# Performance work log

Hardware: AMD Instinct MI355X
Metric: run time of the kernel (lower is better)

The kernel has to match this reference:

```python
import jax, jax.numpy as jnp
from jax import lax
import numpy as np

K_SIZE = 3  # SteerableKernelBase.create_radial(3)


def _radial_basis_3x3():
    """Orthonormal radial steerable basis on a 3x3 grid.
    Returns 6 unit-norm kernels: [k0_center, k0_ring, k1_cos, k1_sin, k2_cos, k2_sin]."""
    ys, xs = np.mgrid[-1:2, -1:2].astype(np.float32)
    ang = np.arctan2(ys, xs)
    ring = (np.hypot(xs, ys) > 0).astype(np.float32)

    def unit(k):
        return (k / np.linalg.norm(k)).astype(np.float32)

    b0c = np.zeros((3, 3), np.float32); b0c[1, 1] = 1.0
    basis = np.stack([
        b0c,                       # k=0, r=0
        unit(ring),                # k=0, r=1
        unit(np.cos(ang) * ring),  # k=1 real
        unit(np.sin(ang) * ring),  # k=1 imag
        unit(np.cos(2 * ang) * ring),  # k=2 real
        unit(np.sin(2 * ang) * ring),  # k=2 imag
    ])
    return jnp.asarray(basis)  # (6, 3, 3)


def setup_inputs() -> dict:
    key = jax.random.key(0)
    k1, k2, k3 = jax.random.split(key, 3)
    N, C_in, C_out, H, W = 16, 64, 64, 128, 128
    x = jax.random.normal(k1, (N, C_in, H, W), dtype=jnp.float32)
    # steering angle field in [0,1); alpha = (cos 2*pi*theta, sin 2*pi*theta) is unitary
    theta = jax.random.uniform(k2, (N, 1, H, W), dtype=jnp.float32)
    # steerable weights: (n_out, n_in, 4) -> [k0 center, k0 ring, k1, k2]
    fan_in = C_in * K_SIZE * K_SIZE
    std = jnp.sqrt(2.0 / fan_in)  # relu gain init as in steerable_base.init_weights
    weights = jax.random.normal(k3, (C_out, C_in, 4), dtype=jnp.float32) * std
    bias = jnp.zeros((C_out,), dtype=jnp.float32)
    return {"x": x, "theta": theta, "weights": weights, "bias": bias}


def reference(x, theta, weights, bias):
    basis = _radial_basis_3x3()  # (6,3,3)
    O = weights.shape[0]
    w = weights[..., None, None]  # (O,I,4,1,1)
    # Synthesize per-harmonic kernels (O,I,3,3) from the steerable basis
    k0 = w[:, :, 0] * basis[0] + w[:, :, 1] * basis[1]
    k1r = w[:, :, 2] * basis[2]
    k1i = w[:, :, 2] * basis[3]
    k2r = w[:, :, 3] * basis[4]
    k2i = w[:, :, 3] * basis[5]
    ker = jnp.concatenate([k0, k1r, k1i, k2r, k2i], axis=0)  # (5O, I, 3, 3)

    z = lax.conv_general_dilated(
        x, ker, window_strides=(1, 1), padding="SAME",
        dimension_numbers=("NCHW", "OIHW", "NCHW"))  # (N, 5O, H, W)
    N, _, H, W = z.shape
    z = z.reshape(N, 5, O, H, W)

    # angle harmonics cos(k*alpha), sin(k*alpha); alpha unitary so rho=1 path
    a = 2.0 * jnp.pi * theta  # (N,1,H,W)
    c1, s1 = jnp.cos(a), jnp.sin(a)
    c2 = 2.0 * c1 * c1 - 1.0
    s2 = 2.0 * s1 * c1

    out = (z[:, 0] + c1 * z[:, 1] + s1 * z[:, 2]
           + c2 * z[:, 3] + s2 * z[:, 4])
    return out + bias[None, :, None, None]
```

## Files before the change

### kernel.cpp

```cpp
#include <hip/hip_runtime.h>


typedef __bf16 bf16x8 __attribute__((ext_vector_type(8)));
typedef float  f32x16 __attribute__((ext_vector_type(16)));
typedef float  f32x4  __attribute__((ext_vector_type(4)));
typedef unsigned int u32;
typedef const __attribute__((address_space(1))) u32* gp_t;
typedef __attribute__((address_space(3))) u32* lp_t;

#define HH 128
#define WW 128
#define CHCH 8
#define NCHUNK 8
#define NBUF 3
#define RROWS 10
#define RCOLS 40
#define CHF 400
#define CHIMG 65536

__global__ void wt_repack(const float* __restrict__ wt,
                          unsigned short* __restrict__ wb) {
    int i = blockIdx.x * 256 + threadIdx.x;
    int o = i >> 8, k = i & 255;
    union { float f; u32 u; } v; v.f = wt[i];
    unsigned short b = (unsigned short)((v.u + 0x7FFF + ((v.u >> 16) & 1)) >> 16);
    int kcg = k >> 4, hxx = (k >> 3) & 1, r = k & 7;
    wb[((kcg * 2 + hxx) * 64 + o) * 8 + r] = b;
}

__global__ __launch_bounds__(256, 3) void steered_conv_mfma(
    const float* __restrict__ x, const float* __restrict__ theta,
    const unsigned short* __restrict__ wb, const float* __restrict__ bias,
    float* __restrict__ out)
{
    __shared__ __attribute__((aligned(16))) float lds[NBUF][CHCH][CHF];

    const int tid = threadIdx.x;
    const int wid = tid >> 6, lane = tid & 63;
    const int pc = lane & 31, hx = lane >> 5;

    const int bb = blockIdx.x;
    const int swz = (bb & 7) * 128 + (bb >> 3);
    const int n = swz >> 6;
    const int ty = (swz >> 2) & 15, tx = swz & 3;
    const int h0 = ty * 8, w0 = tx * 32;
    const int p0 = wid * 2;

    const int oA = lane * 16;
    const int rA = oA / 160;
    const int cA = oA - rA * 160;
    int ghA = h0 - 1 + rA; ghA = ghA < 0 ? 0 : (ghA > 127 ? 127 : ghA);
    int srcA = ghA * 512 + w0 * 4 - 16 + cA;
    srcA = srcA < 0 ? 0 : srcA;
    const bool skA = (w0 == 0 && cA < 16) || (w0 == 96 && cA >= 144)
                   || (h0 == 0 && rA == 0);

    const int oB = 1024 + lane * 16;
    const int rB = oB / 160;
    const int cB = oB - rB * 160;
    int ghB = h0 - 1 + rB; ghB = ghB < 0 ? 0 : (ghB > 127 ? 127 : ghB);
    int srcB = ghB * 512 + w0 * 4 - 16 + cB;
    srcB = srcB < 0 ? 0 : (srcB > CHIMG - 16 ? CHIMG - 16 : srcB);
    const bool skB = (lane >= 36) || (w0 == 0 && cB < 16) || (w0 == 96 && cB >= 144)
                   || (h0 == 120 && rB == 9);

    const char* xn = (const char*)x + (size_t)n * 64 * CHIMG;

    float s1a, c1a, s1b, c1b;
    __sincosf(6.2831853071795864769f * theta[(n*HH + h0+p0)*WW + w0+pc], &s1a, &c1a);
    __sincosf(6.2831853071795864769f * theta[(n*HH + h0+p0+1)*WW + w0+pc], &s1b, &c1b);
    const float c2a = 2.f*c1a*c1a - 1.f, s2a = 2.f*s1a*c1a;
    const float c2b = 2.f*c1b*c1b - 1.f, s2b = 2.f*s1b*c1b;

    if ((h0 == 0) | (h0 == 120) | (w0 == 0) | (w0 == 96)) {
        f32x4* z = (f32x4*)&lds[0][0][0];
        for (int i = tid; i < NBUF * CHCH * CHF / 4; i += 256)
            z[i] = f32x4{0.f, 0.f, 0.f, 0.f};
    }
    __syncthreads();

    auto stage = [&](int t) {
        const char* xc = xn + (size_t)(t * CHCH) * CHIMG;
        #pragma unroll
        for (int j = 0; j < 2; ++j) {
            const int ch = wid * 2 + j;
            const char* s = xc + ch * CHIMG;
            char* d = (char*)&lds[t % NBUF][ch][0];
            if (!skA) __builtin_amdgcn_global_load_lds((gp_t)(s + srcA), (lp_t)d, 16, 0, 0);
            if (!skB) __builtin_amdgcn_global_load_lds((gp_t)(s + srcB), (lp_t)(d + 1024), 16, 0, 0);
        }
    };

    const unsigned short* wbl = wb + (hx * 64 + pc) * 8;
    bf16x8 wE0, wE1, wE2, wE3, wO0, wO1, wO2, wO3;

    stage(0);
    {
        const unsigned short* wr = wbl;
        wE0 = *(const bf16x8*)(wr);
        wE1 = *(const bf16x8*)(wr + 256);
        wE2 = *(const bf16x8*)(wr + 1024);
        wE3 = *(const bf16x8*)(wr + 1280);
    }
    stage(1);

    f32x16 acc00, acc01, acc10, acc11;
    #pragma unroll
    for (int r = 0; r < 16; ++r) { acc00[r]=0.f; acc01[r]=0.f; acc10[r]=0.f; acc11[r]=0.f; }

    const float RS  = 0.35355339059327373f;
    const float HMR = 0.14644660940672627f;

    #pragma unroll
    for (int c = 0; c < NCHUNK; ++c) {
        if (c == NCHUNK - 1) asm volatile("s_waitcnt vmcnt(0)" ::: "memory");
        else                 asm volatile("s_waitcnt vmcnt(4)" ::: "memory");
        __builtin_amdgcn_sched_barrier(0);
        __builtin_amdgcn_s_barrier();
        if (c + 1 < NCHUNK) {
            const unsigned short* wr = wbl + (c + 1) * 2048;
            if ((c + 1) & 1) {
                wO0 = *(const bf16x8*)(wr);
                wO1 = *(const bf16x8*)(wr + 256);
                wO2 = *(const bf16x8*)(wr + 1024);
                wO3 = *(const bf16x8*)(wr + 1280);
            } else {
                wE0 = *(const bf16x8*)(wr);
                wE1 = *(const bf16x8*)(wr + 256);
                wE2 = *(const bf16x8*)(wr + 1024);
                wE3 = *(const bf16x8*)(wr + 1280);
            }
        }
        if (c + 2 < NCHUNK) stage(c + 2);
        __builtin_amdgcn_sched_barrier(0);

        const bf16x8 A00 = (c & 1) ? wO0 : wE0;
        const bf16x8 A01 = (c & 1) ? wO1 : wE1;
        const bf16x8 A10 = (c & 1) ? wO2 : wE2;
        const bf16x8 A11 = (c & 1) ? wO3 : wE3;

        const float* tb = &lds[c % NBUF][0][p0 * RCOLS + pc + 3];
        #pragma unroll
        for (int kc = 0; kc < 2; ++kc) {
            bf16x8 b0, b1;
            #pragma unroll
            for (int cs = 0; cs < 2; ++cs) {
                const float* t = tb + (kc * 4 + hx * 2 + cs) * CHF;
                const float t00=t[0],   t01=t[1],   t02=t[2];
                const float t10=t[40],  t11=t[41],  t12=t[42];
                const float t20=t[80],  t21=t[81],  t22=t[82];
                const float t30=t[120], t31=t[121], t32=t[122];
                const float S0=t00+t01+t02, S1=t10+t11+t12;
                const float S2=t20+t21+t22, S3=t30+t31+t32;
                const float D0=t02-t00, D1=t12-t10, D2=t22-t20, D3=t32-t30;
                {
                    const float F1 = RS * (S0 + S2 + S1 - t11);
                    const float B2 = RS * (D0 + D2) + 0.5f * D1;
                    const float B3 = RS * (S2 - S0) + HMR * (t21 - t01);
                    const float B4 = 0.5f * (S1 - t11 - t01 - t21);
                    const float B5 = 0.5f * (D2 - D0);
                    b0[cs*4+0] = (__bf16)t11;
                    b0[cs*4+1] = (__bf16)F1;
                    b0[cs*4+2] = (__bf16)(c1a * B2 + s1a * B3);
                    b0[cs*4+3] = (__bf16)(c2a * B4 + s2a * B5);
                }
                {
                    const float F1 = RS * (S1 + S3 + S2 - t21);
                    const float B2 = RS * (D1 + D3) + 0.5f * D2;
                    const float B3 = RS * (S3 - S1) + HMR * (t31 - t11);
                    const float B4 = 0.5f * (S2 - t21 - t11 - t31);
                    const float B5 = 0.5f * (D3 - D1);
                    b1[cs*4+0] = (__bf16)t21;
                    b1[cs*4+1] = (__bf16)F1;
                    b1[cs*4+2] = (__bf16)(c1b * B2 + s1b * B3);
                    b1[cs*4+3] = (__bf16)(c2b * B4 + s2b * B5);
                }
            }
            const bf16x8 A0 = kc ? A10 : A00;
            const bf16x8 A1 = kc ? A11 : A01;
            __builtin_amdgcn_s_setprio(1);
            acc00 = __builtin_amdgcn_mfma_f32_32x32x16_bf16(A0, b0, acc00, 0, 0, 0);
            acc01 = __builtin_amdgcn_mfma_f32_32x32x16_bf16(A1, b0, acc01, 0, 0, 0);
            acc10 = __builtin_amdgcn_mfma_f32_32x32x16_bf16(A0, b1, acc10, 0, 0, 0);
            acc11 = __builtin_amdgcn_mfma_f32_32x32x16_bf16(A1, b1, acc11, 0, 0, 0);
            __builtin_amdgcn_s_setprio(0);
        }
    }

    const size_t hw = (size_t)HH * WW;
    float* op = out + (size_t)n * 64 * hw + (size_t)(h0 + p0) * WW + w0 + pc;
    #pragma unroll
    for (int r = 0; r < 16; ++r) {
        const int o = (r & 3) + 8 * (r >> 2) + 4 * hx;
        const float bo = bias[o], bo2 = bias[o + 32];
        op[(size_t)o * hw]             = acc00[r] + bo;
        op[(size_t)(o + 32) * hw]      = acc01[r] + bo2;
        op[(size_t)o * hw + WW]        = acc10[r] + bo;
        op[(size_t)(o + 32) * hw + WW] = acc11[r] + bo2;
    }
}

extern "C" void kernel_launch(void* const* d_in, const int* in_sizes, int n_in,
                              void* d_out, int out_size, void* d_ws, size_t ws_size,
                              hipStream_t stream) {
    const float* x     = (const float*)d_in[0];
    const float* theta = (const float*)d_in[1];
    const float* wt    = (const float*)d_in[2];
    const float* bias  = (const float*)d_in[3];
    float* out = (float*)d_out;
    unsigned short* wb = (unsigned short*)d_ws;

    wt_repack<<<64, 256, 0, stream>>>(wt, wb);

    steered_conv_mfma<<<1024, 256, 0, stream>>>(x, theta, wb, bias, out);
}
```

Baseline: 41.84 us.

## Use single-wave blocks with private double-buffered LDS, removing block barriers

Measured after the change: 41.03 us. Within noise of the previous version (-1.9%).

```diff
diff --git a/kernel.cpp b/kernel.cpp
--- a/kernel.cpp
+++ b/kernel.cpp
@@ -10,12 +10,7 @@
 
 #define HH 128
 #define WW 128
-#define CHCH 8
-#define NCHUNK 8
-#define NBUF 3
-#define RROWS 10
-#define RCOLS 40
-#define CHF 400
+#define HW 16384
 #define CHIMG 65536
 
 __global__ void wt_repack(const float* __restrict__ wt,
@@ -28,73 +23,72 @@
     wb[((kcg * 2 + hxx) * 64 + o) * 8 + r] = b;
 }
 
-__global__ __launch_bounds__(256, 3) void steered_conv_mfma(
+__global__ __launch_bounds__(64, 3) void steered_conv_mfma(
     const float* __restrict__ x, const float* __restrict__ theta,
     const unsigned short* __restrict__ wb, const float* __restrict__ bias,
     float* __restrict__ out)
 {
-    __shared__ __attribute__((aligned(16))) float lds[NBUF][CHCH][CHF];
-
-    const int tid = threadIdx.x;
-    const int wid = tid >> 6, lane = tid & 63;
+    __shared__ __attribute__((aligned(16))) float xs[2][8][4][40];
+
+    const int lane = threadIdx.x & 63;
     const int pc = lane & 31, hx = lane >> 5;
 
-    const int bb = blockIdx.x;
-    const int swz = (bb & 7) * 128 + (bb >> 3);
-    const int n = swz >> 6;
-    const int ty = (swz >> 2) & 15, tx = swz & 3;
-    const int h0 = ty * 8, w0 = tx * 32;
-    const int p0 = wid * 2;
-
-    const int oA = lane * 16;
-    const int rA = oA / 160;
-    const int cA = oA - rA * 160;
-    int ghA = h0 - 1 + rA; ghA = ghA < 0 ? 0 : (ghA > 127 ? 127 : ghA);
-    int srcA = ghA * 512 + w0 * 4 - 16 + cA;
-    srcA = srcA < 0 ? 0 : srcA;
-    const bool skA = (w0 == 0 && cA < 16) || (w0 == 96 && cA >= 144)
-                   || (h0 == 0 && rA == 0);
-
-    const int oB = 1024 + lane * 16;
-    const int rB = oB / 160;
-    const int cB = oB - rB * 160;
-    int ghB = h0 - 1 + rB; ghB = ghB < 0 ? 0 : (ghB > 127 ? 127 : ghB);
-    int srcB = ghB * 512 + w0 * 4 - 16 + cB;
-    srcB = srcB < 0 ? 0 : (srcB > CHIMG - 16 ? CHIMG - 16 : srcB);
-    const bool skB = (lane >= 36) || (w0 == 0 && cB < 16) || (w0 == 96 && cB >= 144)
-                   || (h0 == 120 && rB == 9);
+    const int bb  = blockIdx.x;
+    const int swz = (bb & 7) * 512 + (bb >> 3);
+    const int n   = swz >> 8;
+    const int rem = swz & 255;
+    const int hA  = (rem >> 2) * 2;
+    const int w0  = (rem & 3) * 32;
+    const int w   = w0 + pc;
+
+    int soff[5];
+    int skip[5];
+    #pragma unroll
+    for (int d = 0; d < 5; ++d) {
+        const int i   = d * 1024 + lane * 16;
+        const int ch  = i / 640;
+        const int rm  = i - ch * 640;
+        const int row = rm / 160;
+        const int c16 = rm - row * 160;
+        const int gh  = hA - 1 + row;
+        const int ghc = gh < 0 ? 0 : (gh > 127 ? 127 : gh);
+        int so = ch * CHIMG + ghc * 512 + w0 * 4 - 16 + c16;
+        soff[d] = so < 0 ? 0 : so;
+        skip[d] = (gh < 0) | (gh > 127) |
+                  ((w0 == 0) & (c16 < 16)) | ((w0 == 96) & (c16 >= 144));
+    }
 
     const char* xn = (const char*)x + (size_t)n * 64 * CHIMG;
 
     float s1a, c1a, s1b, c1b;
-    __sincosf(6.2831853071795864769f * theta[(n*HH + h0+p0)*WW + w0+pc], &s1a, &c1a);
-    __sincosf(6.2831853071795864769f * theta[(n*HH + h0+p0+1)*WW + w0+pc], &s1b, &c1b);
+    __sincosf(6.2831853071795864769f * theta[(n*HH + hA)*WW + w], &s1a, &c1a);
+    __sincosf(6.2831853071795864769f * theta[(n*HH + hA+1)*WW + w], &s1b, &c1b);
     const float c2a = 2.f*c1a*c1a - 1.f, s2a = 2.f*s1a*c1a;
     const float c2b = 2.f*c1b*c1b - 1.f, s2b = 2.f*s1b*c1b;
 
-    if ((h0 == 0) | (h0 == 120) | (w0 == 0) | (w0 == 96)) {
-        f32x4* z = (f32x4*)&lds[0][0][0];
-        for (int i = tid; i < NBUF * CHCH * CHF / 4; i += 256)
-            z[i] = f32x4{0.f, 0.f, 0.f, 0.f};
-    }
-    __syncthreads();
+    if (hA == 0 || hA == 126 || w0 == 0 || w0 == 96) {
+        f32x4* z = (f32x4*)&xs[0][0][0][0];
+        #pragma unroll
+        for (int i = 0; i < 10; ++i)
+            z[lane + i * 64] = f32x4{0.f, 0.f, 0.f, 0.f};
+        asm volatile("s_waitcnt lgkmcnt(0)" ::: "memory");
+    }
 
     auto stage = [&](int t) {
-        const char* xc = xn + (size_t)(t * CHCH) * CHIMG;
+        const char* sb = xn + (size_t)(t * 8) * CHIMG;
+        char* db = (char*)&xs[t & 1][0][0][0];
         #pragma unroll
-        for (int j = 0; j < 2; ++j) {
-            const int ch = wid * 2 + j;
-            const char* s = xc + ch * CHIMG;
-            char* d = (char*)&lds[t % NBUF][ch][0];
-            if (!skA) __builtin_amdgcn_global_load_lds((gp_t)(s + srcA), (lp_t)d, 16, 0, 0);
-            if (!skB) __builtin_amdgcn_global_load_lds((gp_t)(s + srcB), (lp_t)(d + 1024), 16, 0, 0);
-        }
+        for (int d = 0; d < 5; ++d)
+            if (!skip[d])
+                __builtin_amdgcn_global_load_lds((gp_t)(sb + soff[d]),
+                                                 (lp_t)(db + d * 1024), 16, 0, 0);
     };
 
     const unsigned short* wbl = wb + (hx * 64 + pc) * 8;
     bf16x8 wE0, wE1, wE2, wE3, wO0, wO1, wO2, wO3;
 
     stage(0);
+    __builtin_amdgcn_sched_barrier(0);
     {
         const unsigned short* wr = wbl;
         wE0 = *(const bf16x8*)(wr);
@@ -102,7 +96,9 @@
         wE2 = *(const bf16x8*)(wr + 1024);
         wE3 = *(const bf16x8*)(wr + 1280);
     }
+    __builtin_amdgcn_sched_barrier(0);
     stage(1);
+    __builtin_amdgcn_sched_barrier(0);
 
     f32x16 acc00, acc01, acc10, acc11;
     #pragma unroll
@@ -112,12 +108,11 @@
     const float HMR = 0.14644660940672627f;
 
     #pragma unroll
-    for (int c = 0; c < NCHUNK; ++c) {
-        if (c == NCHUNK - 1) asm volatile("s_waitcnt vmcnt(0)" ::: "memory");
-        else                 asm volatile("s_waitcnt vmcnt(4)" ::: "memory");
+    for (int c = 0; c < 8; ++c) {
+        if (c == 7) asm volatile("s_waitcnt vmcnt(0)" ::: "memory");
+        else        asm volatile("s_waitcnt vmcnt(5)" ::: "memory");
         __builtin_amdgcn_sched_barrier(0);
-        __builtin_amdgcn_s_barrier();
-        if (c + 1 < NCHUNK) {
+        if (c < 7) {
             const unsigned short* wr = wbl + (c + 1) * 2048;
             if ((c + 1) & 1) {
                 wO0 = *(const bf16x8*)(wr);
@@ -130,22 +125,21 @@
                 wE2 = *(const bf16x8*)(wr + 1024);
                 wE3 = *(const bf16x8*)(wr + 1280);
             }
+            __builtin_amdgcn_sched_barrier(0);
         }
-        if (c + 2 < NCHUNK) stage(c + 2);
-        __builtin_amdgcn_sched_barrier(0);
 
         const bf16x8 A00 = (c & 1) ? wO0 : wE0;
         const bf16x8 A01 = (c & 1) ? wO1 : wE1;
         const bf16x8 A10 = (c & 1) ? wO2 : wE2;
         const bf16x8 A11 = (c & 1) ? wO3 : wE3;
 
-        const float* tb = &lds[c % NBUF][0][p0 * RCOLS + pc + 3];
+        const float* tb = &xs[c & 1][0][0][0];
         #pragma unroll
         for (int kc = 0; kc < 2; ++kc) {
             bf16x8 b0, b1;
             #pragma unroll
             for (int cs = 0; cs < 2; ++cs) {
-                const float* t = tb + (kc * 4 + hx * 2 + cs) * CHF;
+                const float* t = tb + (kc * 4 + hx * 2 + cs) * 160 + pc + 3;
                 const float t00=t[0],   t01=t[1],   t02=t[2];
                 const float t10=t[40],  t11=t[41],  t12=t[42];
                 const float t20=t[80],  t21=t[81],  t22=t[82];
@@ -185,10 +179,14 @@
             acc11 = __builtin_amdgcn_mfma_f32_32x32x16_bf16(A1, b1, acc11, 0, 0, 0);
             __builtin_amdgcn_s_setprio(0);
         }
-    }
-
-    const size_t hw = (size_t)HH * WW;
-    float* op = out + (size_t)n * 64 * hw + (size_t)(h0 + p0) * WW + w0 + pc;
+        asm volatile("s_waitcnt lgkmcnt(0)" ::: "memory");
+        __builtin_amdgcn_sched_barrier(0);
+        if (c < 6) stage(c + 2);
+        __builtin_amdgcn_sched_barrier(0);
+    }
+
+    const size_t hw = (size_t)HW;
+    float* op = out + (size_t)n * 64 * hw + (size_t)hA * WW + w;
     #pragma unroll
     for (int r = 0; r < 16; ++r) {
         const int o = (r & 3) + 8 * (r >> 2) + 4 * hx;
@@ -212,5 +210,5 @@
 
     wt_repack<<<64, 256, 0, stream>>>(wt, wb);
 
-    steered_conv_mfma<<<1024, 256, 0, stream>>>(x, theta, wb, bias, out);
+    steered_conv_mfma<<<4096, 64, 0, stream>>>(x, theta, wb, bias, out);
 }
```
